# Kernel optimization log

Measured on AMD Instinct MI355X. Metric: run time of the kernel, lower is better.

## Reference

```python
import jax, jax.numpy as jnp
import numpy as np

EPS = 1e-8
N_BOX = 524288


def _make_boxes(key, n):
    k1, k2, k3, k4 = jax.random.split(key, 4)
    center = jax.random.uniform(k1, (n, 3), minval=-40.0, maxval=40.0)
    dims = jax.random.uniform(k2, (n, 3), minval=1.0, maxval=4.0)   # h, w, l
    ry = jax.random.uniform(k3, (n, 1), minval=-np.pi, maxval=np.pi)
    return jnp.concatenate([center, dims, ry], axis=1).astype(jnp.float32)


def setup_inputs() -> dict:
    key = jax.random.key(0)
    kg, kq, kp = jax.random.split(key, 3)
    gboxes = _make_boxes(kg, N_BOX)
    # perturb so many pairs actually overlap (realistic proposal-vs-GT setting)
    pert = jax.random.normal(kp, (N_BOX, 7), dtype=jnp.float32) * jnp.array(
        [0.5, 0.2, 0.5, 0.2, 0.2, 0.2, 0.1], dtype=jnp.float32)
    qboxes = gboxes + pert
    return {"gboxes": gboxes, "qboxes": qboxes}


def _bev_corners(boxes):
    # boxes [N,7] = (x,y,z,h,w,l,ry); BEV rect l (x-dir) by w (z-dir), yaw ry
    x, z = boxes[:, 0], boxes[:, 2]
    w, l, ry = boxes[:, 4], boxes[:, 5], boxes[:, 6]
    lx = jnp.array([0.5, 0.5, -0.5, -0.5], boxes.dtype)
    lz = jnp.array([0.5, -0.5, -0.5, 0.5], boxes.dtype)
    cx = lx[None, :] * l[:, None]
    cz = lz[None, :] * w[:, None]
    c, s = jnp.cos(ry)[:, None], jnp.sin(ry)[:, None]
    X = c * cx + s * cz + x[:, None]
    Z = -s * cx + c * cz + z[:, None]
    return jnp.stack([X, Z], axis=-1)  # [N,4,2]


def _cross2(a, b):
    return a[..., 0] * b[..., 1] - a[..., 1] * b[..., 0]


def _inside(pts, boxes):
    # pts [N,4,2] world -> local frame of boxes; inside axis-aligned l x w rect
    x, z = boxes[:, 0, None], boxes[:, 2, None]
    w, l, ry = boxes[:, 4, None], boxes[:, 5, None], boxes[:, 6, None]
    c, s = jnp.cos(ry), jnp.sin(ry)
    rx = pts[..., 0] - x
    rz = pts[..., 1] - z
    lx = c * rx - s * rz
    lz = s * rx + c * rz
    return (jnp.abs(lx) <= 0.5 * l + 1e-5) & (jnp.abs(lz) <= 0.5 * w + 1e-5)


def _bev_inter_area(ca, cb):
    # convex polygon intersection area of two rotated rects, vectorized over N
    # candidate vertices: 16 edge-edge intersections + 4 + 4 contained corners
    a1 = ca[:, :, None, :]                      # [N,4,1,2]
    a2 = jnp.roll(ca, -1, axis=1)[:, :, None, :]
    b1 = cb[:, None, :, :]                      # [N,1,4,2]
    b2 = jnp.roll(cb, -1, axis=1)[:, None, :, :]
    d1, d2 = a2 - a1, b2 - b1
    denom = _cross2(d1, d2)                     # [N,4,4]
    safe = jnp.where(jnp.abs(denom) > EPS, denom, 1.0)
    t = _cross2(b1 - a1, d2) / safe
    u = _cross2(b1 - a1, d1) / safe
    ok = (jnp.abs(denom) > EPS) & (t >= 0) & (t <= 1) & (u >= 0) & (u <= 1)
    ipts = a1 + t[..., None] * d1               # [N,4,4,2]
    n = ca.shape[0]
    pts = jnp.concatenate([ipts.reshape(n, 16, 2), ca, cb], axis=1)   # [N,24,2]
    mask = jnp.concatenate(
        [ok.reshape(n, 16), _inside(ca, None_b := None) if False else _inside_wrap(ca, cb)], axis=1)
    return pts, mask


def _inside_wrap(ca, cb):
    raise NotImplementedError


def _inter_area(ca, cb, ga, qa):
    n = ca.shape[0]
    a1 = ca[:, :, None, :]
    a2 = jnp.roll(ca, -1, axis=1)[:, :, None, :]
    b1 = cb[:, None, :, :]
    b2 = jnp.roll(cb, -1, axis=1)[:, None, :, :]
    d1, d2 = a2 - a1, b2 - b1
    denom = _cross2(d1, d2)
    safe = jnp.where(jnp.abs(denom) > EPS, denom, 1.0)
    t = _cross2(b1 - a1, d2) / safe
    u = _cross2(b1 - a1, d1) / safe
    ok = (jnp.abs(denom) > EPS) & (t >= 0) & (t <= 1) & (u >= 0) & (u <= 1)
    ipts = a1 + t[..., None] * d1
    pts = jnp.concatenate([ipts.reshape(n, 16, 2), ca, cb], axis=1)      # [N,24,2]
    mask = jnp.concatenate([ok.reshape(n, 16),
                            _inside(ca, qa), _inside(cb, ga)], axis=1)   # [N,24]
    cnt = jnp.maximum(mask.sum(axis=1, keepdims=True), 1)
    mean = (pts * mask[..., None]).sum(axis=1, keepdims=True) / cnt[..., None]
    rel = pts - mean
    ang = jnp.where(mask, jnp.arctan2(rel[..., 1], rel[..., 0]), 1e9)
    order = jnp.argsort(ang, axis=1)
    pts_s = jnp.take_along_axis(pts, order[..., None], axis=1)
    mask_s = jnp.take_along_axis(mask, order, axis=1)
    # invalid slots collapse onto first (valid) vertex -> zero shoelace terms
    pts_s = jnp.where(mask_s[..., None], pts_s, pts_s[:, :1, :])
    nxt = jnp.roll(pts_s, -1, axis=1)
    area = 0.5 * jnp.abs(_cross2(pts_s, nxt).sum(axis=1))
    return area


def _iou3d(gboxes, qboxes):
    ca, cb = _bev_corners(gboxes), _bev_corners(qboxes)
    area = _inter_area(ca, cb, gboxes, qboxes)
    # vertical (y) overlap: box spans [y - h, y]
    ya, ha = gboxes[:, 1], gboxes[:, 3]
    yb, hb = qboxes[:, 1], qboxes[:, 3]
    h_ov = jnp.maximum(jnp.minimum(ya, yb) - jnp.maximum(ya - ha, yb - hb), 0.0)
    inter = area * h_ov
    vol_a = gboxes[:, 3] * gboxes[:, 4] * gboxes[:, 5]
    vol_b = qboxes[:, 3] * qboxes[:, 4] * qboxes[:, 5]
    iou = inter / (vol_a + vol_b - inter + EPS)
    return jnp.clip(iou, 0.0, 1.0)


def reference(gboxes, qboxes):
    ious = _iou3d(gboxes, qboxes)
    return jnp.mean(1.0 - ious)
```

## Files before the change

### kernel.cpp

```cpp
#include <hip/hip_runtime.h>
#include <math.h>

#define EPS_F 1e-8f
#define POISON_U32 0xAAAAAAAAu
#define GRP_SHIFT 5
#define GRP_SIZE  32
#define BLK 256
#define BPT 4
#define BOXES (BLK * BPT)
#define CHUNK (BOXES * 7)

__device__ __forceinline__ float rcp_fast(float x) { return __builtin_amdgcn_rcpf(x); }

__launch_bounds__(BLK)
__global__ void iou3d_fused_kernel(const float* __restrict__ g,
                                   const float* __restrict__ q,
                                   float* __restrict__ out,
                                   unsigned char* __restrict__ ws,
                                   int n, int nblocks, float invn) {
    const int tid = threadIdx.x;
    const int grp = blockIdx.x >> GRP_SHIFT;
    unsigned* gcnt = (unsigned*)(ws + (size_t)grp * 128);
    unsigned* lvl2 = (unsigned*)(ws + 8192);
    float* partial = (float*)(ws + 8448);
    float* gpart   = (float*)(ws + 8448 + (size_t)nblocks * 4);

    if (tid == 0) {
        unsigned v = __hip_atomic_load(gcnt, __ATOMIC_RELAXED, __HIP_MEMORY_SCOPE_AGENT);
        if (v == POISON_U32) {
            unsigned exp = POISON_U32;
            __hip_atomic_compare_exchange_strong(gcnt, &exp, 0u, __ATOMIC_RELAXED,
                                                 __ATOMIC_RELAXED, __HIP_MEMORY_SCOPE_AGENT);
        }
    }

    __shared__ float sgb[CHUNK];
    __shared__ float sqb[CHUNK];
    const size_t elemBase = (size_t)blockIdx.x * CHUNK;
    const long long availll = (long long)n * 7 - (long long)elemBase;
    if (availll >= CHUNK) {
        const float4* g4 = (const float4*)(g + elemBase);
        const float4* q4 = (const float4*)(q + elemBase);
#pragma unroll
        for (int k = 0; k < CHUNK / 4 / BLK; ++k) {
            const int i = tid + k * BLK;
            ((float4*)sgb)[i] = g4[i];
            ((float4*)sqb)[i] = q4[i];
        }
    } else {
        const int avail = (int)availll;
        for (int i = tid; i < avail; i += BLK) {
            sgb[i] = g[elemBase + i];
            sqb[i] = q[elemBase + i];
        }
    }
    __syncthreads();

    float loss = 0.0f;
#pragma unroll
    for (int b = 0; b < BPT; ++b) {
        const int bi = tid + b * BLK;
        const int gid = blockIdx.x * BOXES + bi;
        if (gid >= n) continue;
        const float* gb = sgb + bi * 7;
        const float* qb = sqb + bi * 7;
        const float gx = gb[0], gy = gb[1], gz = gb[2], gh = gb[3], gw = gb[4], gl = gb[5], gr = gb[6];
        const float qx = qb[0], qy = qb[1], qz = qb[2], qh = qb[3], qw = qb[4], ql = qb[5], qr = qb[6];

        float sg, cg, sq_, cq;
        __sincosf(gr, &sg, &cg);
        __sincosf(qr, &sq_, &cq);

        const float LX[4] = {0.5f, 0.5f, -0.5f, -0.5f};
        const float LZ[4] = {0.5f, -0.5f, -0.5f, 0.5f};
        const float dqx = qx - gx, dqz = qz - gz;
        float ax[4], az[4], bx[4], bz[4];
#pragma unroll
        for (int k = 0; k < 4; ++k) {
            const float cxg = LX[k] * gl, czg = LZ[k] * gw;
            ax[k] =  cg * cxg + sg * czg;
            az[k] = -sg * cxg + cg * czg;
            const float cxq = LX[k] * ql, czq = LZ[k] * qw;
            bx[k] =  cq * cxq + sq_ * czq + dqx;
            bz[k] = -sq_ * cxq + cq * czq + dqz;
        }

        float aex[4], aez[4], acc_[4], bex[4], bez[4], bcc[4];
#pragma unroll
        for (int k = 0; k < 4; ++k) {
            aex[k] = ax[(k + 1) & 3] - ax[k];
            aez[k] = az[(k + 1) & 3] - az[k];
            acc_[k] = aex[k] * az[k] - aez[k] * ax[k];
            bex[k] = bx[(k + 1) & 3] - bx[k];
            bez[k] = bz[(k + 1) & 3] - bz[k];
            bcc[k] = bex[k] * bz[k] - bez[k] * bx[k];
        }

        float sm[4][4], rr[4][4];
#pragma unroll
        for (int k = 0; k < 4; ++k)
#pragma unroll
            for (int h = 0; h < 4; ++h) {
                sm[k][h] = bex[h] * aez[k] - bez[h] * aex[k];
                rr[k][h] = rcp_fast(sm[k][h]);
            }

        float total = 0.0f;

#pragma unroll
        for (int k = 0; k < 4; ++k) {
            const float Px = ax[k], Pz = az[k];
            float t0 = 0.0f, t1 = 1.0f;
#pragma unroll
            for (int h = 0; h < 4; ++h) {
                const float s  = sm[k][h];
                const float f0 = bex[h] * Pz - bez[h] * Px - bcc[h];
                const float tt = -f0 * rr[k][h];
                t1 = fminf(t1, (s >= 0.0f) ? tt : 1e30f);
                t0 = fmaxf(t0, (s >= 0.0f) ? -1e30f : tt);
            }
            total += fmaxf(t1 - t0, 0.0f) * (-acc_[k]);
        }
#pragma unroll
        for (int h = 0; h < 4; ++h) {
            const float Px = bx[h], Pz = bz[h];
            float t0 = 0.0f, t1 = 1.0f;
#pragma unroll
            for (int k = 0; k < 4; ++k) {
                const float smv = sm[k][h];
                const float f0 = aex[k] * Pz - aez[k] * Px - acc_[k];
                const float tt = f0 * rr[k][h];
                t1 = fminf(t1, (smv < 0.0f) ? tt : 1e30f);
                t0 = fmaxf(t0, (smv < 0.0f) ? -1e30f : tt);
            }
            total += fmaxf(t1 - t0, 0.0f) * (-bcc[h]);
        }

        const float area = 0.5f * fabsf(total);

        const float hov = fmaxf(fminf(gy, qy) - fmaxf(gy - gh, qy - qh), 0.0f);
        const float inter = area * hov;
        const float va = gh * gw * gl;
        const float vb = qh * qw * ql;
        float iou = inter / (va + vb - inter + EPS_F);
        iou = fminf(fmaxf(iou, 0.0f), 1.0f);
        loss += 1.0f - iou;
    }

#pragma unroll
    for (int off = 32; off > 0; off >>= 1) loss += __shfl_down(loss, off, 64);
    __shared__ float wsum[4];
    __shared__ int roleSh;
    __shared__ int finalSh;
    const int lane = tid & 63;
    const int wid = tid >> 6;
    if (lane == 0) wsum[wid] = loss;
    __syncthreads();

    const int gbase = grp * GRP_SIZE;
    const int gsz = min(GRP_SIZE, nblocks - gbase);
    const int ngroups = (nblocks + GRP_SIZE - 1) >> GRP_SHIFT;

    if (tid == 0) {
        const float bs = wsum[0] + wsum[1] + wsum[2] + wsum[3];
        __hip_atomic_store(&partial[blockIdx.x], bs, __ATOMIC_RELAXED, __HIP_MEMORY_SCOPE_AGENT);
        asm volatile("s_waitcnt vmcnt(0)" ::: "memory");
        const unsigned t = __hip_atomic_fetch_add(gcnt, 1u, __ATOMIC_RELAXED, __HIP_MEMORY_SCOPE_AGENT);
        roleSh = (t + 1u == (unsigned)gsz) ? 1 : 0;
        if (roleSh)
            __hip_atomic_store(gcnt, 0u, __ATOMIC_RELAXED, __HIP_MEMORY_SCOPE_AGENT);
        finalSh = 0;
    }
    __syncthreads();

    if (roleSh) {
        if (tid < GRP_SIZE) {
            float v = (tid < gsz)
                ? __hip_atomic_load(&partial[gbase + tid], __ATOMIC_RELAXED, __HIP_MEMORY_SCOPE_AGENT)
                : 0.f;
#pragma unroll
            for (int off = 16; off > 0; off >>= 1) v += __shfl_down(v, off, 32);
            if (tid == 0) {
                __hip_atomic_store(&gpart[grp], v, __ATOMIC_RELAXED, __HIP_MEMORY_SCOPE_AGENT);
                asm volatile("s_waitcnt vmcnt(0)" ::: "memory");
                unsigned w = __hip_atomic_load(lvl2, __ATOMIC_RELAXED, __HIP_MEMORY_SCOPE_AGENT);
                if (w == POISON_U32) {
                    unsigned exp = POISON_U32;
                    __hip_atomic_compare_exchange_strong(lvl2, &exp, 0u, __ATOMIC_RELAXED,
                                                         __ATOMIC_RELAXED, __HIP_MEMORY_SCOPE_AGENT);
                }
                const unsigned u = __hip_atomic_fetch_add(lvl2, 1u, __ATOMIC_RELAXED,
                                                          __HIP_MEMORY_SCOPE_AGENT);
                if (u + 1u == (unsigned)ngroups) {
                    __hip_atomic_store(lvl2, 0u, __ATOMIC_RELAXED, __HIP_MEMORY_SCOPE_AGENT);
                    finalSh = 1;
                }
            }
        }
        __syncthreads();
        if (finalSh && tid == 0) {
            float v = 0.f;
            for (int j = 0; j < ngroups; ++j)
                v += __hip_atomic_load(&gpart[j], __ATOMIC_RELAXED, __HIP_MEMORY_SCOPE_AGENT);
            out[0] = v * invn;
        }
    }
}

extern "C" void kernel_launch(void* const* d_in, const int* in_sizes, int n_in,
                              void* d_out, int out_size, void* d_ws, size_t ws_size,
                              hipStream_t stream) {
    const float* g = (const float*)d_in[0];
    const float* q = (const float*)d_in[1];
    float* out = (float*)d_out;
    const int n = in_sizes[0] / 7;
    const int nblocks = (n + BOXES - 1) / BOXES;
    iou3d_fused_kernel<<<nblocks, BLK, 0, stream>>>(g, q, out, (unsigned char*)d_ws,
                                                    n, nblocks, 1.0f / (float)n);
}
```

Baseline: 18.94 us.

## Compute BEV intersection via slab clipping in each box's local frame

```diff
diff --git a/kernel.cpp b/kernel.cpp
--- a/kernel.cpp
+++ b/kernel.cpp
@@ -11,6 +11,17 @@
 #define CHUNK (BOXES * 7)
 
 __device__ __forceinline__ float rcp_fast(float x) { return __builtin_amdgcn_rcpf(x); }
+
+__device__ __forceinline__ float clip_len(float Px, float Pz, float rdx, float rdz,
+                                          float hx, float hz) {
+    const float tx0 = (-hx - Px) * rdx;
+    const float tx1 = ( hx - Px) * rdx;
+    const float tz0 = (-hz - Pz) * rdz;
+    const float tz1 = ( hz - Pz) * rdz;
+    const float t0 = fmaxf(fmaxf(fminf(tx0, tx1), fminf(tz0, tz1)), 0.0f);
+    const float t1 = fminf(fminf(fmaxf(tx0, tx1), fmaxf(tz0, tz1)), 1.0f);
+    return fmaxf(t1 - t0, 0.0f);
+}
 
 __launch_bounds__(BLK)
 __global__ void iou3d_fused_kernel(const float* __restrict__ g,
@@ -71,76 +82,67 @@
         __sincosf(gr, &sg, &cg);
         __sincosf(qr, &sq_, &cq);
 
-        const float LX[4] = {0.5f, 0.5f, -0.5f, -0.5f};
-        const float LZ[4] = {0.5f, -0.5f, -0.5f, 0.5f};
+        const float hla = 0.5f * gl, hwa = 0.5f * gw;
+        const float hlq = 0.5f * ql, hwq = 0.5f * qw;
+
+        const float cr = cg * cq + sg * sq_;
+        const float sr = sg * cq - cg * sq_;
         const float dqx = qx - gx, dqz = qz - gz;
-        float ax[4], az[4], bx[4], bz[4];
-#pragma unroll
-        for (int k = 0; k < 4; ++k) {
-            const float cxg = LX[k] * gl, czg = LZ[k] * gw;
-            ax[k] =  cg * cxg + sg * czg;
-            az[k] = -sg * cxg + cg * czg;
-            const float cxq = LX[k] * ql, czq = LZ[k] * qw;
-            bx[k] =  cq * cxq + sq_ * czq + dqx;
-            bz[k] = -sq_ * cxq + cq * czq + dqz;
-        }
-
-        float aex[4], aez[4], acc_[4], bex[4], bez[4], bcc[4];
-#pragma unroll
-        for (int k = 0; k < 4; ++k) {
-            aex[k] = ax[(k + 1) & 3] - ax[k];
-            aez[k] = az[(k + 1) & 3] - az[k];
-            acc_[k] = aex[k] * az[k] - aez[k] * ax[k];
-            bex[k] = bx[(k + 1) & 3] - bx[k];
-            bez[k] = bz[(k + 1) & 3] - bz[k];
-            bcc[k] = bex[k] * bz[k] - bez[k] * bx[k];
-        }
-
-        float sm[4][4], rr[4][4];
-#pragma unroll
-        for (int k = 0; k < 4; ++k)
-#pragma unroll
-            for (int h = 0; h < 4; ++h) {
-                sm[k][h] = bex[h] * aez[k] - bez[h] * aex[k];
-                rr[k][h] = rcp_fast(sm[k][h]);
-            }
+
+        const float Tx = cg * dqx - sg * dqz;
+        const float Tz = sg * dqx + cg * dqz;
+        const float E1x = cr * hlq,  E1z = sr * hlq;
+        const float E2x = -sr * hwq, E2z = cr * hwq;
+        const float q0x = Tx + E1x + E2x, q0z = Tz + E1z + E2z;
+        const float q1x = Tx + E1x - E2x, q1z = Tz + E1z - E2z;
+        const float q2x = Tx - E1x - E2x, q2z = Tz - E1z - E2z;
+        const float q3x = Tx - E1x + E2x, q3z = Tz - E1z + E2z;
+        const float F1x = E1x + E1x, F1z = E1z + E1z;
+        const float F2x = E2x + E2x, F2z = E2z + E2z;
+        const float rF1x = rcp_fast(F1x), rF1z = rcp_fast(F1z);
+        const float rF2x = rcp_fast(F2x), rF2z = rcp_fast(F2z);
 
         float total = 0.0f;
-
-#pragma unroll
-        for (int k = 0; k < 4; ++k) {
-            const float Px = ax[k], Pz = az[k];
-            float t0 = 0.0f, t1 = 1.0f;
-#pragma unroll
-            for (int h = 0; h < 4; ++h) {
-                const float s  = sm[k][h];
-                const float f0 = bex[h] * Pz - bez[h] * Px - bcc[h];
-                const float tt = -f0 * rr[k][h];
-                t1 = fminf(t1, (s >= 0.0f) ? tt : 1e30f);
-                t0 = fmaxf(t0, (s >= 0.0f) ? -1e30f : tt);
-            }
-            total += fmaxf(t1 - t0, 0.0f) * (-acc_[k]);
-        }
-#pragma unroll
-        for (int h = 0; h < 4; ++h) {
-            const float Px = bx[h], Pz = bz[h];
-            float t0 = 0.0f, t1 = 1.0f;
-#pragma unroll
-            for (int k = 0; k < 4; ++k) {
-                const float smv = sm[k][h];
-                const float f0 = aex[k] * Pz - aez[k] * Px - acc_[k];
-                const float tt = f0 * rr[k][h];
-                t1 = fminf(t1, (smv < 0.0f) ? tt : 1e30f);
-                t0 = fmaxf(t0, (smv < 0.0f) ? -1e30f : tt);
-            }
-            total += fmaxf(t1 - t0, 0.0f) * (-bcc[h]);
-        }
-
-        const float area = 0.5f * fabsf(total);
+        {
+            const float l0 = clip_len(q0x, q0z, -rF2x, -rF2z, hla, hwa);
+            const float c0 = q0x * F2z - q0z * F2x;
+            total = fmaf(l0, -c0, total);
+            const float l1 = clip_len(q1x, q1z, -rF1x, -rF1z, hla, hwa);
+            const float c1 = q1x * F1z - q1z * F1x;
+            total = fmaf(l1, -c1, total);
+            const float l2 = clip_len(q2x, q2z,  rF2x,  rF2z, hla, hwa);
+            const float c2 = q2x * F2z - q2z * F2x;
+            total = fmaf(l2, c2, total);
+            const float l3 = clip_len(q3x, q3z,  rF1x,  rF1z, hla, hwa);
+            const float c3 = q3x * F1z - q3z * F1x;
+            total = fmaf(l3, c3, total);
+        }
+
+        const float Ux = -(cq * dqx - sq_ * dqz);
+        const float Uz = -(sq_ * dqx + cq * dqz);
+        const float G1x = cr * hla,  G1z = -sr * hla;
+        const float G2x = sr * hwa,  G2z = cr * hwa;
+        const float p0x = Ux + G1x + G2x, p0z = Uz + G1z + G2z;
+        const float p1x = Ux + G1x - G2x, p1z = Uz + G1z - G2z;
+        const float p2x = Ux - G1x - G2x, p2z = Uz - G1z - G2z;
+        const float p3x = Ux - G1x + G2x, p3z = Uz - G1z + G2z;
+        const float H1x = G1x + G1x, H1z = G1z + G1z;
+        const float H2x = G2x + G2x, H2z = G2z + G2z;
+        const float rH1x = rcp_fast(H1x), rH1z = rcp_fast(H1z);
+        const float rH2x = rcp_fast(H2x), rH2z = rcp_fast(H2z);
+
+        const float m0 = clip_len(p0x, p0z, -rH2x, -rH2z, hlq, hwq);
+        const float m1 = clip_len(p1x, p1z, -rH1x, -rH1z, hlq, hwq);
+        const float m2 = clip_len(p2x, p2z,  rH2x,  rH2z, hlq, hwq);
+        const float m3 = clip_len(p3x, p3z,  rH1x,  rH1z, hlq, hwq);
+        const float glw = gl * gw;
+        total = fmaf((m0 + m1) + (m2 + m3), -0.5f * glw, total);
+
+        const float area2 = fabsf(total);
 
         const float hov = fmaxf(fminf(gy, qy) - fmaxf(gy - gh, qy - qh), 0.0f);
-        const float inter = area * hov;
-        const float va = gh * gw * gl;
+        const float inter = 0.5f * area2 * hov;
+        const float va = gh * glw;
         const float vb = qh * qw * ql;
         float iou = inter / (va + vb - inter + EPS_F);
         iou = fminf(fmaxf(iou, 0.0f), 1.0f);
```

Measured after the change: 15.60 us (median of 2 runs). 1.21x faster.
